# Kernel tuning notes

Measured on AMD Instinct MI355X. Metric: run time of the kernel, lower is better.

Reference implementation:

```python
import jax, jax.numpy as jnp
import numpy as np

N_NODES = 100000
MAX_DEG = 64
NODE_DIM = 256
V = 8192
NUM_SAMPLES = 16


def setup_inputs() -> dict:
    key = jax.random.key(0)
    k1, k2, k3, k4 = jax.random.split(key, 4)
    ids = jax.random.randint(k1, (V,), 0, N_NODES, dtype=jnp.int32)
    adj_info = jax.random.randint(k2, (N_NODES, MAX_DEG), 0, N_NODES, dtype=jnp.int32)
    features = jax.random.normal(k3, (N_NODES, NODE_DIM), dtype=jnp.float32)
    W = jax.random.normal(k4, (NODE_DIM, NODE_DIM), dtype=jnp.float32) * 0.05
    b = jnp.zeros((NODE_DIM,), dtype=jnp.float32)
    return {"ids": ids, "adj_info": adj_info, "features": features, "W": W, "b": b,
            "num_samples": NUM_SAMPLES}


def reference(ids, adj_info, features, W, b, num_samples):
    n_nodes, neig_num = adj_info.shape
    group_dim = neig_num // num_samples
    K = group_dim * num_samples  # tf.slice to a multiple of num_samples
    v = ids.shape[0]

    adj_lists = adj_info[ids][:, :K]                     # [V, K] neighbor ids
    v_f = features[ids]                                  # [V, d]
    n_f = features[adj_lists]                            # [V, K, d]

    # linear sampler branch: dense(v_f) then matmul with neighbor feats, relu
    l = v_f @ W + b                                      # [V, d]
    scores = jax.nn.relu(jnp.einsum('vd,vkd->vk', l, n_f))  # [V, K]

    # grouped argmin: pick one neighbor per group of group_dim
    scores = scores.reshape(v, num_samples, group_dim)   # [V, S, G]
    idx_y = jnp.argmin(scores, axis=-1).astype(jnp.int32)  # [V, S]
    idx_y = idx_y + (jnp.arange(num_samples, dtype=jnp.int32) * group_dim)[None, :]

    sel = jnp.take_along_axis(adj_lists, idx_y, axis=1)  # [V, S]

    # count non-padding neighbors (padding sentinel = n_nodes - 1)
    nonpad = jnp.where(sel == n_nodes - 1,
                       jnp.zeros(sel.shape, jnp.float32),
                       jnp.ones(sel.shape, jnp.float32))
    numnz = nonpad.sum(axis=1)                           # [V]
    att = jnp.ones(sel.shape, jnp.float32)
    return sel, att, numnz, numnz
```

## Files before the change

kernel.cpp:

```cpp
#include <hip/hip_runtime.h>
#include <hip/hip_bf16.h>

#define N_NODES   100000
#define MAX_DEG   64
#define NODE_DIM  256
#define NUM_V     8192
#define NSAMP     16
#define GROUP_DIM 4
#define SENTINEL  (N_NODES - 1)

#define BM 64
#define BN 64
#define BK 32
#define AS_STRIDE (BM + 4)

__global__ __launch_bounds__(256) void gemm_l_kernel(
    const int* __restrict__ ids,
    const float* __restrict__ features,
    const float* __restrict__ W,
    const float* __restrict__ bias,
    float* __restrict__ l_out) {
  __shared__ float As[BK][AS_STRIDE];
  __shared__ float Ws[BK][BN];
  __shared__ int   nid_s[BM];

  const int tid  = threadIdx.x;
  const int row0 = blockIdx.x * BM;
  const int col0 = blockIdx.y * BN;

  if (tid < BM) nid_s[tid] = ids[row0 + tid];
  __syncthreads();

  const int tx = tid & 15;
  const int ty = tid >> 4;

  const int am = tid >> 2;
  const int ak = (tid & 3) * 4;
  const int wk = tid >> 4;
  const int wn = (tid & 15) * 4;

  const size_t a_base = (size_t)nid_s[am] * NODE_DIM + ak;
  const size_t w_base = (size_t)wk * NODE_DIM + col0 + wn;

  float4 av0, av1, wv0, wv1;
  av0 = *reinterpret_cast<const float4*>(&features[a_base]);
  av1 = *reinterpret_cast<const float4*>(&features[a_base + 16]);
  wv0 = *reinterpret_cast<const float4*>(&W[w_base]);
  wv1 = *reinterpret_cast<const float4*>(&W[w_base + 16 * NODE_DIM]);

  float acc[4][4] = {};

  for (int k0 = 0; k0 < NODE_DIM; k0 += BK) {
    As[ak + 0][am] = av0.x;
    As[ak + 1][am] = av0.y;
    As[ak + 2][am] = av0.z;
    As[ak + 3][am] = av0.w;
    As[ak + 16 + 0][am] = av1.x;
    As[ak + 16 + 1][am] = av1.y;
    As[ak + 16 + 2][am] = av1.z;
    As[ak + 16 + 3][am] = av1.w;
    *reinterpret_cast<float4*>(&Ws[wk][wn])      = wv0;
    *reinterpret_cast<float4*>(&Ws[wk + 16][wn]) = wv1;
    __syncthreads();

    if (k0 + BK < NODE_DIM) {
      const int kn = k0 + BK;
      av0 = *reinterpret_cast<const float4*>(&features[a_base + kn]);
      av1 = *reinterpret_cast<const float4*>(&features[a_base + kn + 16]);
      wv0 = *reinterpret_cast<const float4*>(&W[w_base + (size_t)kn * NODE_DIM]);
      wv1 = *reinterpret_cast<const float4*>(
          &W[w_base + (size_t)(kn + 16) * NODE_DIM]);
    }

#pragma unroll
    for (int k = 0; k < BK; ++k) {
      const float4 ra = *reinterpret_cast<const float4*>(&As[k][ty * 4]);
      const float4 rb = *reinterpret_cast<const float4*>(&Ws[k][tx * 4]);
      const float a[4] = {ra.x, ra.y, ra.z, ra.w};
      const float b[4] = {rb.x, rb.y, rb.z, rb.w};
#pragma unroll
      for (int i = 0; i < 4; ++i)
#pragma unroll
        for (int j = 0; j < 4; ++j) acc[i][j] += a[i] * b[j];
    }
    __syncthreads();
  }

  const float4 bv = *reinterpret_cast<const float4*>(&bias[col0 + tx * 4]);
#pragma unroll
  for (int i = 0; i < 4; ++i) {
    const int m = row0 + ty * 4 + i;
    float4 o;
    o.x = acc[i][0] + bv.x;
    o.y = acc[i][1] + bv.y;
    o.z = acc[i][2] + bv.z;
    o.w = acc[i][3] + bv.w;
    *reinterpret_cast<float4*>(&l_out[(size_t)m * NODE_DIM + col0 + tx * 4]) = o;
  }
}

__global__ __launch_bounds__(256) void sampler_kernel(
    const int* __restrict__ ids,
    const int* __restrict__ adj,
    const float* __restrict__ features,
    const float* __restrict__ l,
    float* __restrict__ out_sel,
    float* __restrict__ out_att,
    float* __restrict__ out_nz1,
    float* __restrict__ out_nz2) {
  __shared__ float l_s[NODE_DIM];
  __shared__ int   adj_s[MAX_DEG];
  __shared__ float nz_s[NSAMP];

  const int v   = blockIdx.x;
  const int tid = threadIdx.x;
  const int nid = ids[v];

  l_s[tid] = l[(size_t)v * NODE_DIM + tid];
  if (tid < MAX_DEG) adj_s[tid] = adj[(size_t)nid * MAX_DEG + tid];
  __syncthreads();

  const int wave = tid >> 6;
  const int lane = tid & 63;
  const int q    = lane >> 2;
  const int sub  = lane & 3;
  const int k    = wave * 16 + q;

  const int nb = adj_s[k];
  const float* __restrict__ rowp = features + (size_t)nb * NODE_DIM + sub * 4;
  const float* __restrict__ lp   = l_s + sub * 4;

  float p = 0.0f;
#pragma unroll
  for (int c = 0; c < 16; ++c) {
    const float4 f  = *reinterpret_cast<const float4*>(rowp + c * 16);
    const float4 lv = *reinterpret_cast<const float4*>(lp + c * 16);
    p += f.x * lv.x + f.y * lv.y + f.z * lv.z + f.w * lv.w;
  }
  p += __shfl_xor(p, 1, 64);
  p += __shfl_xor(p, 2, 64);
  float s = p > 0.0f ? p : 0.0f;

  int g = q & 3;
  {
    float os = __shfl_xor(s, 4, 64);
    int   og = __shfl_xor(g, 4, 64);
    if (os < s || (os == s && og < g)) { s = os; g = og; }
    os = __shfl_xor(s, 8, 64);
    og = __shfl_xor(g, 8, 64);
    if (os < s || (os == s && og < g)) { s = os; g = og; }
  }

  if ((lane & 15) == 0) {
    const int gl    = lane >> 4;
    const int s_idx = wave * 4 + gl;
    const int selid = adj_s[s_idx * GROUP_DIM + g];
    out_sel[(size_t)v * NSAMP + s_idx] = (float)selid;
    out_att[(size_t)v * NSAMP + s_idx] = 1.0f;
    nz_s[s_idx] = (selid == SENTINEL) ? 0.0f : 1.0f;
  }
  __syncthreads();

  if (tid == 0) {
    float nz = 0.0f;
#pragma unroll
    for (int t = 0; t < NSAMP; ++t) nz += nz_s[t];
    out_nz1[v] = nz;
    out_nz2[v] = nz;
  }
}

extern "C" void kernel_launch(void* const* d_in, const int* in_sizes, int n_in,
                              void* d_out, int out_size, void* d_ws,
                              size_t ws_size, hipStream_t stream) {
  const int*   ids      = (const int*)d_in[0];
  const int*   adj      = (const int*)d_in[1];
  const float* features = (const float*)d_in[2];
  const float* W        = (const float*)d_in[3];
  const float* bias     = (const float*)d_in[4];

  float* l_ws = (float*)d_ws;

  float* out     = (float*)d_out;
  float* out_sel = out;
  float* out_att = out + (size_t)NUM_V * NSAMP;
  float* out_nz1 = out + (size_t)2 * NUM_V * NSAMP;
  float* out_nz2 = out_nz1 + NUM_V;

  gemm_l_kernel<<<dim3(NUM_V / BM, NODE_DIM / BN), 256, 0, stream>>>(
      ids, features, W, bias, l_ws);
  sampler_kernel<<<NUM_V, 256, 0, stream>>>(ids, adj, features, l_ws, out_sel,
                                            out_att, out_nz1, out_nz2);
}
```

Baseline: 235.5 us.

## Fuse dense projection into sampler kernel as per-node GEMV

After: 282.2 us. 1.2x slower.

```diff
diff --git a/kernel.cpp b/kernel.cpp
--- a/kernel.cpp
+++ b/kernel.cpp
@@ -9,105 +9,17 @@
 #define GROUP_DIM 4
 #define SENTINEL  (N_NODES - 1)
 
-#define BM 64
-#define BN 64
-#define BK 32
-#define AS_STRIDE (BM + 4)
-
-__global__ __launch_bounds__(256) void gemm_l_kernel(
+__global__ __launch_bounds__(256) void fused_sampler_kernel(
     const int* __restrict__ ids,
+    const int* __restrict__ adj,
     const float* __restrict__ features,
     const float* __restrict__ W,
     const float* __restrict__ bias,
-    float* __restrict__ l_out) {
-  __shared__ float As[BK][AS_STRIDE];
-  __shared__ float Ws[BK][BN];
-  __shared__ int   nid_s[BM];
-
-  const int tid  = threadIdx.x;
-  const int row0 = blockIdx.x * BM;
-  const int col0 = blockIdx.y * BN;
-
-  if (tid < BM) nid_s[tid] = ids[row0 + tid];
-  __syncthreads();
-
-  const int tx = tid & 15;
-  const int ty = tid >> 4;
-
-  const int am = tid >> 2;
-  const int ak = (tid & 3) * 4;
-  const int wk = tid >> 4;
-  const int wn = (tid & 15) * 4;
-
-  const size_t a_base = (size_t)nid_s[am] * NODE_DIM + ak;
-  const size_t w_base = (size_t)wk * NODE_DIM + col0 + wn;
-
-  float4 av0, av1, wv0, wv1;
-  av0 = *reinterpret_cast<const float4*>(&features[a_base]);
-  av1 = *reinterpret_cast<const float4*>(&features[a_base + 16]);
-  wv0 = *reinterpret_cast<const float4*>(&W[w_base]);
-  wv1 = *reinterpret_cast<const float4*>(&W[w_base + 16 * NODE_DIM]);
-
-  float acc[4][4] = {};
-
-  for (int k0 = 0; k0 < NODE_DIM; k0 += BK) {
-    As[ak + 0][am] = av0.x;
-    As[ak + 1][am] = av0.y;
-    As[ak + 2][am] = av0.z;
-    As[ak + 3][am] = av0.w;
-    As[ak + 16 + 0][am] = av1.x;
-    As[ak + 16 + 1][am] = av1.y;
-    As[ak + 16 + 2][am] = av1.z;
-    As[ak + 16 + 3][am] = av1.w;
-    *reinterpret_cast<float4*>(&Ws[wk][wn])      = wv0;
-    *reinterpret_cast<float4*>(&Ws[wk + 16][wn]) = wv1;
-    __syncthreads();
-
-    if (k0 + BK < NODE_DIM) {
-      const int kn = k0 + BK;
-      av0 = *reinterpret_cast<const float4*>(&features[a_base + kn]);
-      av1 = *reinterpret_cast<const float4*>(&features[a_base + kn + 16]);
-      wv0 = *reinterpret_cast<const float4*>(&W[w_base + (size_t)kn * NODE_DIM]);
-      wv1 = *reinterpret_cast<const float4*>(
-          &W[w_base + (size_t)(kn + 16) * NODE_DIM]);
-    }
-
-#pragma unroll
-    for (int k = 0; k < BK; ++k) {
-      const float4 ra = *reinterpret_cast<const float4*>(&As[k][ty * 4]);
-      const float4 rb = *reinterpret_cast<const float4*>(&Ws[k][tx * 4]);
-      const float a[4] = {ra.x, ra.y, ra.z, ra.w};
-      const float b[4] = {rb.x, rb.y, rb.z, rb.w};
-#pragma unroll
-      for (int i = 0; i < 4; ++i)
-#pragma unroll
-        for (int j = 0; j < 4; ++j) acc[i][j] += a[i] * b[j];
-    }
-    __syncthreads();
-  }
-
-  const float4 bv = *reinterpret_cast<const float4*>(&bias[col0 + tx * 4]);
-#pragma unroll
-  for (int i = 0; i < 4; ++i) {
-    const int m = row0 + ty * 4 + i;
-    float4 o;
-    o.x = acc[i][0] + bv.x;
-    o.y = acc[i][1] + bv.y;
-    o.z = acc[i][2] + bv.z;
-    o.w = acc[i][3] + bv.w;
-    *reinterpret_cast<float4*>(&l_out[(size_t)m * NODE_DIM + col0 + tx * 4]) = o;
-  }
-}
-
-__global__ __launch_bounds__(256) void sampler_kernel(
-    const int* __restrict__ ids,
-    const int* __restrict__ adj,
-    const float* __restrict__ features,
-    const float* __restrict__ l,
     float* __restrict__ out_sel,
     float* __restrict__ out_att,
     float* __restrict__ out_nz1,
     float* __restrict__ out_nz2) {
+  __shared__ float f_s[NODE_DIM];
   __shared__ float l_s[NODE_DIM];
   __shared__ int   adj_s[MAX_DEG];
   __shared__ float nz_s[NSAMP];
@@ -116,8 +28,18 @@
   const int tid = threadIdx.x;
   const int nid = ids[v];
 
-  l_s[tid] = l[(size_t)v * NODE_DIM + tid];
+  f_s[tid] = features[(size_t)nid * NODE_DIM + tid];
   if (tid < MAX_DEG) adj_s[tid] = adj[(size_t)nid * MAX_DEG + tid];
+  __syncthreads();
+
+  {
+    float acc = 0.0f;
+#pragma unroll 8
+    for (int k = 0; k < NODE_DIM; ++k) {
+      acc += f_s[k] * W[(size_t)k * NODE_DIM + tid];
+    }
+    l_s[tid] = acc + bias[tid];
+  }
   __syncthreads();
 
   const int wave = tid >> 6;
@@ -179,16 +101,12 @@
   const float* W        = (const float*)d_in[3];
   const float* bias     = (const float*)d_in[4];
 
-  float* l_ws = (float*)d_ws;
-
   float* out     = (float*)d_out;
   float* out_sel = out;
   float* out_att = out + (size_t)NUM_V * NSAMP;
   float* out_nz1 = out + (size_t)2 * NUM_V * NSAMP;
   float* out_nz2 = out_nz1 + NUM_V;
 
-  gemm_l_kernel<<<dim3(NUM_V / BM, NODE_DIM / BN), 256, 0, stream>>>(
-      ids, features, W, bias, l_ws);
-  sampler_kernel<<<NUM_V, 256, 0, stream>>>(ids, adj, features, l_ws, out_sel,
-                                            out_att, out_nz1, out_nz2);
+  fused_sampler_kernel<<<NUM_V, 256, 0, stream>>>(
+      ids, adj, features, W, bias, out_sel, out_att, out_nz1, out_nz2);
 }
```
